# Optimization experiments

Hardware: AMD Instinct MI355X
Metric: run time of the kernel (lower is better)

The kernel has to match this reference:

```python
import jax, jax.numpy as jnp
import numpy as np

B, T, N, F, UNITS = 64, 12, 512, 64, 64

def setup_inputs() -> dict:
    key = jax.random.key(0)
    ks = jax.random.split(key, 9)
    inputs = jax.random.normal(ks[0], (B, T, N, F), dtype=jnp.float32)
    # binary k-hop adjacency mask with self loops (K.to_dense(calculate_adjacency_k(...)))
    A = (jax.random.uniform(ks[1], (N, N)) < 0.05).astype(jnp.float32)
    A = jnp.maximum(A, jnp.eye(N, dtype=jnp.float32))
    W1 = jax.random.normal(ks[2], (T, 1), dtype=jnp.float32) * 0.3
    W2 = jax.random.normal(ks[3], (F, T), dtype=jnp.float32) * 0.1
    W3 = jax.random.normal(ks[4], (F, 1), dtype=jnp.float32) * 0.1
    Ve = jax.random.normal(ks[5], (N, N), dtype=jnp.float32) * 0.05
    be = jax.random.normal(ks[6], (N, N), dtype=jnp.float32) * 0.05
    kernel = jax.random.normal(ks[7], (F, UNITS), dtype=jnp.float32) * 0.1
    bias = jax.random.normal(ks[8], (UNITS,), dtype=jnp.float32) * 0.1
    return {"inputs": inputs, "A": A, "W1": W1, "W2": W2, "W3": W3,
            "Ve": Ve, "be": be, "kernel": kernel, "bias": bias}

def reference(inputs, A, W1, W2, W3, Ve, be, kernel, bias):
    # inputs: (B, T, N, F)
    # lhs: permute->(B,N,F,T), dot W1, squeeze, dot W2 -> (B, N, T)
    r1 = jnp.einsum('btnf,t->bnf', inputs, W1[:, 0])
    lhs = jnp.einsum('bnf,ft->bnt', r1, W2)
    # rhs: dot W3, squeeze -> (B, T, N)
    rhs = jnp.einsum('btnf,f->btn', inputs, W3[:, 0])
    # batch_dot -> (B, N, N)
    product = jnp.einsum('bnt,btm->bnm', lhs, rhs)
    E = jnp.einsum('jk,bkm->bjm', Ve, jax.nn.sigmoid(product + be))
    masked = E + (-1e16) * (1.0 - A)            # adjacency mask
    attn = jax.nn.softmax(masked, axis=-1)       # (B, N, N)
    # graph conv: (B,N,N) x (B,T,N,F) -> (B,T,N,F)
    conv = jnp.einsum('bjk,btkf->btjf', attn, inputs)
    out = jnp.einsum('btjf,fu->btju', conv, kernel) + bias
    return out  # activation=None -> linear
```

## Files before the change

### kernel.cpp

```cpp
#include <hip/hip_runtime.h>
#include <hip/hip_bf16.h>
#include <cstdint>

constexpr int BB = 64;
constexpr int TT = 12;
constexpr int NN = 512;
constexpr int FF = 64;
constexpr int UU = 64;
constexpr int MAXNZ = 128;

constexpr size_t OF_LHS   = 0;
constexpr size_t OF_RHS   = 393216;
constexpr size_t OF_BET   = 786432;
constexpr size_t OF_EVALS = 1048576;
constexpr size_t OB_NNZ   = 20971520;
constexpr size_t OB_CIDX  = 20973568;
constexpr size_t OB_CCNT  = 21235712;
constexpr size_t OB_COLJ  = 21237760;
constexpr size_t OB_XT    = 21516288;
constexpr size_t XT_BYTES = (size_t)BB * NN * TT * FF * 2;
constexpr size_t OB_KF    = 71847936;
constexpr size_t KF_BYTES = 8 * 64 * 8 * 2;
constexpr size_t OB_VEB   = 71856128;
constexpr size_t VEB_BYTES = (size_t)NN * NN * 2;

typedef __attribute__((ext_vector_type(8))) short bf16x8;
typedef __attribute__((ext_vector_type(4))) float f32x4;

__device__ __forceinline__ float wred_sum(float v) {
  #pragma unroll
  for (int off = 32; off; off >>= 1) v += __shfl_xor(v, off, 64);
  return v;
}

__device__ __forceinline__ float bflo(unsigned u) {
  return __uint_as_float(u << 16);
}
__device__ __forceinline__ float bfhi(unsigned u) {
  return __uint_as_float(u & 0xFFFF0000u);
}

__global__ __launch_bounds__(256) void k_lhs_rhs(
    const float* __restrict__ x, const float* __restrict__ W1,
    const float* __restrict__ W2, const float* __restrict__ W3,
    float* __restrict__ lhs, float* __restrict__ rhsS,
    unsigned short* __restrict__ xT)
{
  int unit = blockIdx.x * 4 + (threadIdx.x >> 6);
  int lane = threadIdx.x & 63;
  int b = unit >> 9, n = unit & 511;

  const float* xb = x + ((size_t)b * TT * NN + n) * FF + lane;
  float xv[12];
  #pragma unroll
  for (int t = 0; t < 12; ++t) xv[t] = xb[(size_t)t * NN * FF];

  if (xT) {
    unsigned short* xo = xT + (size_t)unit * (TT * FF) + lane;
    #pragma unroll
    for (int t = 0; t < 12; ++t) {
      __hip_bfloat16 h = __float2bfloat16(xv[t]);
      xo[t * FF] = *reinterpret_cast<unsigned short*>(&h);
    }
  }

  float r1 = 0.f;
  #pragma unroll
  for (int t = 0; t < 12; ++t) r1 += xv[t] * W1[t];

  float w3 = W3[lane];

  float myl = 0.f, myr = 0.f;
  #pragma unroll
  for (int t = 0; t < 12; ++t) {
    float a = r1 * W2[lane * 12 + t];
    float c = xv[t] * w3;
    a = wred_sum(a);
    c = wred_sum(c);
    if (lane == t) { myl = a; myr = c; }
  }
  if (lane < 12) {
    lhs[(size_t)unit * 12 + lane]  = myl;
    rhsS[(size_t)unit * 12 + lane] = myr;
  }
}

__global__ __launch_bounds__(256) void k_transpose(
    const float* __restrict__ be, float* __restrict__ beT,
    const float* __restrict__ K, unsigned short* __restrict__ KF,
    const float* __restrict__ Ve, unsigned short* __restrict__ VeB)
{
  int bid = blockIdx.x;
  if (bid < NN * NN / 256) {
    int i = bid * 256 + threadIdx.x;
    int k = i >> 9, m = i & 511;
    beT[m * 512 + k] = be[i];
    return;
  }
  if (bid == NN * NN / 256) {
    if (KF) {
      for (int idx = threadIdx.x; idx < 512; idx += 256) {
        int frag = idx >> 6, l = idx & 63;
        int kk = frag >> 2, nt = frag & 3;
        int u = nt * 16 + (l & 15);
        unsigned short* dst = KF + (size_t)idx * 8;
        for (int e = 0; e < 8; ++e) {
          int f = kk * 32 + (l >> 4) * 8 + e;
          __hip_bfloat16 h = __float2bfloat16(K[f * 64 + u]);
          dst[e] = *reinterpret_cast<unsigned short*>(&h);
        }
      }
    }
    return;
  }
  if (VeB) {
    int b2 = bid - (NN * NN / 256 + 1);
    #pragma unroll
    for (int i = 0; i < 32; ++i) {
      int idx = b2 * 8192 + i * 256 + threadIdx.x;
      __hip_bfloat16 h = __float2bfloat16(Ve[idx]);
      VeB[idx] = *reinterpret_cast<unsigned short*>(&h);
    }
  }
}

__global__ void k_build_idx(const float* __restrict__ A,
                            int* __restrict__ nnz, int* __restrict__ cidx)
{
  int j = blockIdx.x;
  int lane = threadIdx.x;
  unsigned long long lt = (1ull << lane) - 1ull;
  int base = 0;
  for (int c = 0; c < 8; ++c) {
    int m = c * 64 + lane;
    bool p = A[(size_t)j * 512 + m] > 0.5f;
    unsigned long long mask = __ballot(p);
    int pos = base + __popcll(mask & lt);
    if (p && pos < MAXNZ) cidx[j * MAXNZ + pos] = m;
    base += __popcll(mask);
  }
  if (lane == 0) nnz[j] = base > MAXNZ ? MAXNZ : base;
}

__global__ void k_build_col(const int* __restrict__ nnz, const int* __restrict__ cidx,
                            int* __restrict__ ccnt, unsigned* __restrict__ colj)
{
  int j = blockIdx.x;
  int lane = threadIdx.x;
  int cnt = nnz[j];
  for (int s = lane; s < cnt; s += 64) {
    int m = cidx[j * MAXNZ + s];
    int pos = atomicAdd(&ccnt[m], 1);
    if (pos < MAXNZ) colj[m * MAXNZ + pos] = (unsigned)j | ((unsigned)s << 16);
  }
}

__global__ __launch_bounds__(256) void k_product_E6(
    const float* __restrict__ lhs, const float* __restrict__ rhsS,
    const float* __restrict__ beT, const unsigned short* __restrict__ VeB,
    const int* __restrict__ ccnt, const unsigned* __restrict__ colj,
    float* __restrict__ evals)
{
  int b  = blockIdx.x;
  int mc = blockIdx.y;

  __shared__ __align__(16) float sL[8][512];
  __shared__ float rh[8 * 12];

  int tid = threadIdx.x;
  int wave = tid >> 6, lane = tid & 63;
  int grp = lane >> 4, lg = lane & 15;

  float l0[12], l1[12];
  {
    const float* p0 = lhs + ((size_t)b * 512 + tid) * 12;
    const float* p1 = p0 + 256 * 12;
    #pragma unroll
    for (int t = 0; t < 12; ++t) { l0[t] = p0[t]; l1[t] = p1[t]; }
  }
  if (tid < 96) rh[tid] = rhsS[((size_t)b * 512 + mc * 8) * 12 + tid];
  __syncthreads();

  #pragma unroll
  for (int mm = 0; mm < 8; ++mm) {
    int m = mc * 8 + mm;
    float q0 = beT[m * 512 + tid];
    float q1 = beT[m * 512 + tid + 256];
    const float* rw = &rh[mm * 12];
    #pragma unroll
    for (int t = 0; t < 12; ++t) {
      q0 = fmaf(l0[t], rw[t], q0);
      q1 = fmaf(l1[t], rw[t], q1);
    }
    sL[mm][tid]       = 1.0f / (1.0f + __expf(-q0));
    sL[mm][tid + 256] = 1.0f / (1.0f + __expf(-q1));
  }
  __syncthreads();

  for (int cc = 0; cc < 2; ++cc) {
    int mm = wave + cc * 4;
    int m = mc * 8 + mm;
    int cnt = ccnt[m];
    if (cnt > MAXNZ) cnt = MAXNZ;
    const float4* sw4 = (const float4*)sL[mm];
    const unsigned* cj = colj + m * MAXNZ;

    int e0 = grp;
    for (; e0 + 4 < cnt; e0 += 8) {
      unsigned pk0 = cj[e0], pk1 = cj[e0 + 4];
      int j0 = pk0 & 0xffff, s0 = (int)(pk0 >> 16);
      int j1 = pk1 & 0xffff, s1 = (int)(pk1 >> 16);
      const uint2* va = (const uint2*)(VeB + (size_t)j0 * 512);
      const uint2* vb = (const uint2*)(VeB + (size_t)j1 * 512);
      float a = 0.f, c = 0.f;
      #pragma unroll
      for (int i = 0; i < 8; ++i) {
        float4 s4 = sw4[lg + 16 * i];
        uint2  u0 = va[lg + 16 * i];
        uint2  u1 = vb[lg + 16 * i];
        a = fmaf(bflo(u0.x), s4.x, a); a = fmaf(bfhi(u0.x), s4.y, a);
        a = fmaf(bflo(u0.y), s4.z, a); a = fmaf(bfhi(u0.y), s4.w, a);
        c = fmaf(bflo(u1.x), s4.x, c); c = fmaf(bfhi(u1.x), s4.y, c);
        c = fmaf(bflo(u1.y), s4.z, c); c = fmaf(bfhi(u1.y), s4.w, c);
      }
      #pragma unroll
      for (int off = 8; off; off >>= 1) {
        a += __shfl_xor(a, off, 64);
        c += __shfl_xor(c, off, 64);
      }
      if (lg == 0) {
        evals[((size_t)b * 512 + j0) * MAXNZ + s0] = a;
        evals[((size_t)b * 512 + j1) * MAXNZ + s1] = c;
      }
    }
    if (e0 < cnt) {
      unsigned pk0 = cj[e0];
      int j0 = pk0 & 0xffff, s0 = (int)(pk0 >> 16);
      const uint2* va = (const uint2*)(VeB + (size_t)j0 * 512);
      float a = 0.f;
      #pragma unroll
      for (int i = 0; i < 8; ++i) {
        float4 s4 = sw4[lg + 16 * i];
        uint2  u0 = va[lg + 16 * i];
        a = fmaf(bflo(u0.x), s4.x, a); a = fmaf(bfhi(u0.x), s4.y, a);
        a = fmaf(bflo(u0.y), s4.z, a); a = fmaf(bfhi(u0.y), s4.w, a);
      }
      #pragma unroll
      for (int off = 8; off; off >>= 1) a += __shfl_xor(a, off, 64);
      if (lg == 0) evals[((size_t)b * 512 + j0) * MAXNZ + s0] = a;
    }
  }
}

__global__ __launch_bounds__(256) void k_product_E5(
    const float* __restrict__ lhs, const float* __restrict__ rhsS,
    const float* __restrict__ beT, const float* __restrict__ Ve,
    const int* __restrict__ ccnt, const unsigned* __restrict__ colj,
    float* __restrict__ evals)
{
  int b  = blockIdx.x;
  int mc = blockIdx.y;

  __shared__ __align__(16) float sL[8][512];
  __shared__ float rh[8 * 12];

  int tid = threadIdx.x;
  int wave = tid >> 6, lane = tid & 63;
  int grp = lane >> 4, lg = lane & 15;

  float l0[12], l1[12];
  {
    const float* p0 = lhs + ((size_t)b * 512 + tid) * 12;
    const float* p1 = p0 + 256 * 12;
    #pragma unroll
    for (int t = 0; t < 12; ++t) { l0[t] = p0[t]; l1[t] = p1[t]; }
  }
  if (tid < 96) rh[tid] = rhsS[((size_t)b * 512 + mc * 8) * 12 + tid];
  __syncthreads();

  #pragma unroll
  for (int mm = 0; mm < 8; ++mm) {
    int m = mc * 8 + mm;
    float q0 = beT[m * 512 + tid];
    float q1 = beT[m * 512 + tid + 256];
    const float* rw = &rh[mm * 12];
    #pragma unroll
    for (int t = 0; t < 12; ++t) {
      q0 = fmaf(l0[t], rw[t], q0);
      q1 = fmaf(l1[t], rw[t], q1);
    }
    sL[mm][tid]       = 1.0f / (1.0f + __expf(-q0));
    sL[mm][tid + 256] = 1.0f / (1.0f + __expf(-q1));
  }
  __syncthreads();

  for (int cc = 0; cc < 2; ++cc) {
    int mm = wave + cc * 4;
    int m = mc * 8 + mm;
    int cnt = ccnt[m];
    if (cnt > MAXNZ) cnt = MAXNZ;
    const float4* sw4 = (const float4*)sL[mm];
    const unsigned* cj = colj + m * MAXNZ;

    int e0 = grp;
    for (; e0 + 4 < cnt; e0 += 8) {
      unsigned pk0 = cj[e0], pk1 = cj[e0 + 4];
      int j0 = pk0 & 0xffff, s0 = (int)(pk0 >> 16);
      int j1 = pk1 & 0xffff, s1 = (int)(pk1 >> 16);
      const float4* va = (const float4*)(Ve + (size_t)j0 * 512);
      const float4* vb = (const float4*)(Ve + (size_t)j1 * 512);
      float a = 0.f, c = 0.f;
      #pragma unroll
      for (int i = 0; i < 8; ++i) {
        float4 s4 = sw4[lg + 16 * i];
        float4 v4 = va[lg + 16 * i];
        float4 w4 = vb[lg + 16 * i];
        a = fmaf(v4.x, s4.x, a); a = fmaf(v4.y, s4.y, a);
        a = fmaf(v4.z, s4.z, a); a = fmaf(v4.w, s4.w, a);
        c = fmaf(w4.x, s4.x, c); c = fmaf(w4.y, s4.y, c);
        c = fmaf(w4.z, s4.z, c); c = fmaf(w4.w, s4.w, c);
      }
      #pragma unroll
      for (int off = 8; off; off >>= 1) {
        a += __shfl_xor(a, off, 64);
        c += __shfl_xor(c, off, 64);
      }
      if (lg == 0) {
        evals[((size_t)b * 512 + j0) * MAXNZ + s0] = a;
        evals[((size_t)b * 512 + j1) * MAXNZ + s1] = c;
      }
    }
    if (e0 < cnt) {
      unsigned pk0 = cj[e0];
      int j0 = pk0 & 0xffff, s0 = (int)(pk0 >> 16);
      const float4* va = (const float4*)(Ve + (size_t)j0 * 512);
      float a = 0.f;
      #pragma unroll
      for (int i = 0; i < 8; ++i) {
        float4 s4 = sw4[lg + 16 * i];
        float4 v4 = va[lg + 16 * i];
        a = fmaf(v4.x, s4.x, a); a = fmaf(v4.y, s4.y, a);
        a = fmaf(v4.z, s4.z, a); a = fmaf(v4.w, s4.w, a);
      }
      #pragma unroll
      for (int off = 8; off; off >>= 1) a += __shfl_xor(a, off, 64);
      if (lg == 0) evals[((size_t)b * 512 + j0) * MAXNZ + s0] = a;
    }
  }
}

__global__ __launch_bounds__(256) void k_out12(
    const unsigned short* __restrict__ xT,
    const int* __restrict__ nnz, const int* __restrict__ cidx,
    const float* __restrict__ evals,
    const unsigned short* __restrict__ KF, const float* __restrict__ bias,
    float* __restrict__ out)
{
  int tid = threadIdx.x;
  int wv = tid >> 6, lane = tid & 63;
  int bid = blockIdx.x;
  int sbid = (bid & 7) * 1024 + (bid >> 3);
  int unit = sbid * 4 + wv;
  int b = unit >> 9, j = unit & 511;

  __shared__ unsigned short convB[4][16][80];
  __shared__ float valL[4][MAXNZ];
  __shared__ int   idxL[4][MAXNZ];

  int cnt = nnz[j];
  for (int s = lane; s < cnt; s += 64) {
    idxL[wv][s] = cidx[j * MAXNZ + s];
    valL[wv][s] = evals[(size_t)unit * MAXNZ + s];
  }
  {
    float v0 = lane < cnt        ? valL[wv][lane]      : -__builtin_inff();
    float v1 = (lane + 64) < cnt ? valL[wv][lane + 64] : -__builtin_inff();
    float mx = fmaxf(v0, v1);
    #pragma unroll
    for (int off = 32; off; off >>= 1) mx = fmaxf(mx, __shfl_xor(mx, off, 64));
    float e0 = lane < cnt        ? __expf(v0 - mx) : 0.f;
    float e1 = (lane + 64) < cnt ? __expf(v1 - mx) : 0.f;
    float ssum = wred_sum(e0 + e1);
    float inv = 1.0f / ssum;
    if (lane < cnt)        valL[wv][lane]      = e0 * inv;
    if ((lane + 64) < cnt) valL[wv][lane + 64] = e1 * inv;
  }

  float2 acc[6];
  #pragma unroll
  for (int i = 0; i < 6; ++i) acc[i] = make_float2(0.f, 0.f);

  const unsigned* xb = reinterpret_cast<const unsigned*>(
      xT + (size_t)b * NN * (TT * FF));

  int s = 0;
  for (; s + 1 < cnt; s += 2) {
    int   k0 = idxL[wv][s],     k1 = idxL[wv][s + 1];
    float v0 = valL[wv][s],     v1 = valL[wv][s + 1];
    const unsigned* p0 = xb + k0 * 384 + lane;
    const unsigned* p1 = xb + k1 * 384 + lane;
    unsigned a0 = p0[0],   a1 = p0[64],  a2 = p0[128],
             a3 = p0[192], a4 = p0[256], a5 = p0[320];
    unsigned c0 = p1[0],   c1 = p1[64],  c2 = p1[128],
             c3 = p1[192], c4 = p1[256], c5 = p1[320];
    acc[0].x = fmaf(v0, bflo(a0), acc[0].x); acc[0].y = fmaf(v0, bfhi(a0), acc[0].y);
    acc[1].x = fmaf(v0, bflo(a1), acc[1].x); acc[1].y = fmaf(v0, bfhi(a1), acc[1].y);
    acc[2].x = fmaf(v0, bflo(a2), acc[2].x); acc[2].y = fmaf(v0, bfhi(a2), acc[2].y);
    acc[3].x = fmaf(v0, bflo(a3), acc[3].x); acc[3].y = fmaf(v0, bfhi(a3), acc[3].y);
    acc[4].x = fmaf(v0, bflo(a4), acc[4].x); acc[4].y = fmaf(v0, bfhi(a4), acc[4].y);
    acc[5].x = fmaf(v0, bflo(a5), acc[5].x); acc[5].y = fmaf(v0, bfhi(a5), acc[5].y);
    acc[0].x = fmaf(v1, bflo(c0), acc[0].x); acc[0].y = fmaf(v1, bfhi(c0), acc[0].y);
    acc[1].x = fmaf(v1, bflo(c1), acc[1].x); acc[1].y = fmaf(v1, bfhi(c1), acc[1].y);
    acc[2].x = fmaf(v1, bflo(c2), acc[2].x); acc[2].y = fmaf(v1, bfhi(c2), acc[2].y);
    acc[3].x = fmaf(v1, bflo(c3), acc[3].x); acc[3].y = fmaf(v1, bfhi(c3), acc[3].y);
    acc[4].x = fmaf(v1, bflo(c4), acc[4].x); acc[4].y = fmaf(v1, bfhi(c4), acc[4].y);
    acc[5].x = fmaf(v1, bflo(c5), acc[5].x); acc[5].y = fmaf(v1, bfhi(c5), acc[5].y);
  }
  if (s < cnt) {
    int   k0 = idxL[wv][s];
    float v0 = valL[wv][s];
    const unsigned* p0 = xb + k0 * 384 + lane;
    unsigned a0 = p0[0],   a1 = p0[64],  a2 = p0[128],
             a3 = p0[192], a4 = p0[256], a5 = p0[320];
    acc[0].x = fmaf(v0, bflo(a0), acc[0].x); acc[0].y = fmaf(v0, bfhi(a0), acc[0].y);
    acc[1].x = fmaf(v0, bflo(a1), acc[1].x); acc[1].y = fmaf(v0, bfhi(a1), acc[1].y);
    acc[2].x = fmaf(v0, bflo(a2), acc[2].x); acc[2].y = fmaf(v0, bfhi(a2), acc[2].y);
    acc[3].x = fmaf(v0, bflo(a3), acc[3].x); acc[3].y = fmaf(v0, bfhi(a3), acc[3].y);
    acc[4].x = fmaf(v0, bflo(a4), acc[4].x); acc[4].y = fmaf(v0, bfhi(a4), acc[4].y);
    acc[5].x = fmaf(v0, bflo(a5), acc[5].x); acc[5].y = fmaf(v0, bfhi(a5), acc[5].y);
  }

  int half = lane >> 5, fl = lane & 31;
  {
    unsigned short* cb = &convB[wv][0][0];
    #pragma unroll
    for (int i = 0; i < 6; ++i) {
      int t = 2 * i + half;
      __hip_bfloat16 hx = __float2bfloat16(acc[i].x);
      __hip_bfloat16 hy = __float2bfloat16(acc[i].y);
      unsigned pkd = (unsigned)*reinterpret_cast<unsigned short*>(&hx)
                   | ((unsigned)*reinterpret_cast<unsigned short*>(&hy) << 16);
      *reinterpret_cast<unsigned*>(&cb[t * 80 + fl * 2]) = pkd;
    }
  }

  int arow = lane & 15, agrp = lane >> 4;
  bf16x8 afrag0 = *reinterpret_cast<const bf16x8*>(&convB[wv][arow][agrp * 8]);
  bf16x8 afrag1 = *reinterpret_cast<const bf16x8*>(&convB[wv][arow][32 + agrp * 8]);
  const bf16x8* kf = reinterpret_cast<const bf16x8*>(KF);

  #pragma unroll
  for (int nt = 0; nt < 4; ++nt) {
    f32x4 accT = {0.f, 0.f, 0.f, 0.f};
    accT = __builtin_amdgcn_mfma_f32_16x16x32_bf16(afrag0, kf[(0 * 4 + nt) * 64 + lane], accT, 0, 0, 0);
    accT = __builtin_amdgcn_mfma_f32_16x16x32_bf16(afrag1, kf[(1 * 4 + nt) * 64 + lane], accT, 0, 0, 0);
    int u = nt * 16 + arow;
    float bb = bias[u];
    #pragma unroll
    for (int r = 0; r < 4; ++r) {
      int t = agrp * 4 + r;
      if (t < 12)
        out[((size_t)(b * TT + t) * NN + j) * UU + u] = accT[r] + bb;
    }
  }
}

__global__ __launch_bounds__(256) void k_out3f(
    const float* __restrict__ x,
    const int* __restrict__ nnz, const int* __restrict__ cidx,
    const float* __restrict__ evals,
    const float* __restrict__ K, const float* __restrict__ bias,
    float* __restrict__ out)
{
  int wv = threadIdx.x >> 6, lane = threadIdx.x & 63;
  int bid = blockIdx.x;
  int sbid = (bid & 7) * 1024 + (bid >> 3);
  int unit = sbid * 4 + wv;
  int b = unit >> 9, j = unit & 511;

  __shared__ float convL[4][12][64];
  __shared__ float valL[4][MAXNZ];
  __shared__ int   idxL[4][MAXNZ];

  int cnt = nnz[j];
  for (int s = lane; s < cnt; s += 64) {
    idxL[wv][s] = cidx[j * MAXNZ + s];
    valL[wv][s] = evals[(size_t)unit * MAXNZ + s];
  }
  {
    float v0 = lane < cnt        ? valL[wv][lane]      : -__builtin_inff();
    float v1 = (lane + 64) < cnt ? valL[wv][lane + 64] : -__builtin_inff();
    float mx = fmaxf(v0, v1);
    #pragma unroll
    for (int off = 32; off; off >>= 1) mx = fmaxf(mx, __shfl_xor(mx, off, 64));
    float e0 = lane < cnt        ? __expf(v0 - mx) : 0.f;
    float e1 = (lane + 64) < cnt ? __expf(v1 - mx) : 0.f;
    float ssum = wred_sum(e0 + e1);
    float inv = 1.0f / ssum;
    if (lane < cnt)        valL[wv][lane]      = e0 * inv;
    if ((lane + 64) < cnt) valL[wv][lane + 64] = e1 * inv;
  }

  float acc[12];
  #pragma unroll
  for (int t = 0; t < 12; ++t) acc[t] = 0.f;

  const float* xb = x + (size_t)b * TT * NN * FF + lane;
  for (int s = 0; s < cnt; ++s) {
    float v = valL[wv][s];
    const float* xk = xb + (size_t)idxL[wv][s] * FF;
    #pragma unroll
    for (int t = 0; t < 12; ++t)
      acc[t] = fmaf(v, xk[(size_t)t * NN * FF], acc[t]);
  }
  #pragma unroll
  for (int t = 0; t < 12; ++t) convL[wv][t][lane] = acc[t];

  float bs = bias[lane];
  float o[12];
  #pragma unroll
  for (int t = 0; t < 12; ++t) o[t] = bs;
  __syncthreads();

  #pragma unroll
  for (int ft = 0; ft < 4; ++ft) {
    float kc[16];
    #pragma unroll
    for (int i = 0; i < 16; ++i) kc[i] = K[(ft * 16 + i) * 64 + lane];
    #pragma unroll
    for (int t = 0; t < 12; ++t) {
      const float4* cv = (const float4*)&convL[wv][t][ft * 16];
      float4 c0 = cv[0], c1 = cv[1], c2 = cv[2], c3 = cv[3];
      float o_ = o[t];
      o_ = fmaf(c0.x, kc[0],  o_); o_ = fmaf(c0.y, kc[1],  o_);
      o_ = fmaf(c0.z, kc[2],  o_); o_ = fmaf(c0.w, kc[3],  o_);
      o_ = fmaf(c1.x, kc[4],  o_); o_ = fmaf(c1.y, kc[5],  o_);
      o_ = fmaf(c1.z, kc[6],  o_); o_ = fmaf(c1.w, kc[7],  o_);
      o_ = fmaf(c2.x, kc[8],  o_); o_ = fmaf(c2.y, kc[9],  o_);
      o_ = fmaf(c2.z, kc[10], o_); o_ = fmaf(c2.w, kc[11], o_);
      o_ = fmaf(c3.x, kc[12], o_); o_ = fmaf(c3.y, kc[13], o_);
      o_ = fmaf(c3.z, kc[14], o_); o_ = fmaf(c3.w, kc[15], o_);
      o[t] = o_;
    }
  }

  #pragma unroll
  for (int t = 0; t < 12; ++t)
    out[((size_t)(b * TT + t) * NN + j) * UU + lane] = o[t];
}

extern "C" void kernel_launch(void* const* d_in, const int* in_sizes, int n_in,
                              void* d_out, int out_size, void* d_ws, size_t ws_size,
                              hipStream_t stream)
{
  const float* x    = (const float*)d_in[0];
  const float* A    = (const float*)d_in[1];
  const float* W1   = (const float*)d_in[2];
  const float* W2   = (const float*)d_in[3];
  const float* W3   = (const float*)d_in[4];
  const float* Ve   = (const float*)d_in[5];
  const float* be   = (const float*)d_in[6];
  const float* K    = (const float*)d_in[7];
  const float* bias = (const float*)d_in[8];
  float* out = (float*)d_out;

  char* ws = (char*)d_ws;
  float* lhs   = (float*)ws + OF_LHS;
  float* rhsS  = (float*)ws + OF_RHS;
  float* beT   = (float*)ws + OF_BET;
  float* evals = (float*)ws + OF_EVALS;
  int*      nnz  = (int*)(ws + OB_NNZ);
  int*      cidx = (int*)(ws + OB_CIDX);
  int*      ccnt = (int*)(ws + OB_CCNT);
  unsigned* colj = (unsigned*)(ws + OB_COLJ);
  unsigned short* xT  = (unsigned short*)(ws + OB_XT);
  unsigned short* KF  = (unsigned short*)(ws + OB_KF);
  unsigned short* VeB = (unsigned short*)(ws + OB_VEB);

  const bool use_xt  = ws_size >= OB_KF + KF_BYTES;
  const bool use_veb = ws_size >= OB_VEB + VEB_BYTES;

  hipMemsetAsync(ccnt, 0, NN * sizeof(int), stream);

  k_lhs_rhs<<<dim3(BB * NN / 4), dim3(256), 0, stream>>>(
      x, W1, W2, W3, lhs, rhsS, use_xt ? xT : nullptr);
  k_transpose<<<dim3(NN * NN / 256 + 1 + (use_veb ? 32 : 0)), dim3(256), 0, stream>>>(
      be, beT, K, use_xt ? KF : nullptr, Ve, use_veb ? VeB : nullptr);
  k_build_idx<<<dim3(NN), dim3(64), 0, stream>>>(A, nnz, cidx);
  k_build_col<<<dim3(NN), dim3(64), 0, stream>>>(nnz, cidx, ccnt, colj);
  if (use_veb)
    k_product_E6<<<dim3(BB, NN / 8), dim3(256), 0, stream>>>(lhs, rhsS, beT, VeB, ccnt, colj, evals);
  else
    k_product_E5<<<dim3(BB, NN / 8), dim3(256), 0, stream>>>(lhs, rhsS, beT, Ve, ccnt, colj, evals);
  if (use_xt)
    k_out12<<<dim3(BB * NN / 4), dim3(256), 0, stream>>>(xT, nnz, cidx, evals, KF, bias, out);
  else
    k_out3f<<<dim3(BB * NN / 4), dim3(256), 0, stream>>>(x, nnz, cidx, evals, K, bias, out);
}
```

Before: 218.0 us.

## Split sigmoid and E computation, compute sparse E entries with bf16 MFMA

Replaces the fused product/E kernel with two kernels: one computes sigmoid(lhs·rhs + be) for all batches and writes it as a dense bf16 tensor, and a second computes only the adjacency-masked E entries per column m using bf16 MFMA over gathered Ve rows. The aim is to move the Ve contraction onto matrix cores and reuse each Ve row across all 64 batches within a block. In exchange it writes and rereads a 32 MB intermediate and needs a larger workspace. The path only runs when the workspace is big enough.

```diff
diff --git a/kernel.cpp b/kernel.cpp
--- a/kernel.cpp
+++ b/kernel.cpp
@@ -23,6 +23,8 @@
 constexpr size_t KF_BYTES = 8 * 64 * 8 * 2;
 constexpr size_t OB_VEB   = 71856128;
 constexpr size_t VEB_BYTES = (size_t)NN * NN * 2;
+constexpr size_t OB_ST    = 72380416;
+constexpr size_t ST_BYTES = (size_t)BB * NN * NN * 2;
 
 typedef __attribute__((ext_vector_type(8))) short bf16x8;
 typedef __attribute__((ext_vector_type(4))) float f32x4;
@@ -152,6 +154,115 @@
     int m = cidx[j * MAXNZ + s];
     int pos = atomicAdd(&ccnt[m], 1);
     if (pos < MAXNZ) colj[m * MAXNZ + pos] = (unsigned)j | ((unsigned)s << 16);
+  }
+}
+
+__global__ __launch_bounds__(256) void k_sigmoid2(
+    const float* __restrict__ lhs, const float* __restrict__ rhsS,
+    const float* __restrict__ beT, unsigned short* __restrict__ ST)
+{
+  int b  = blockIdx.x;
+  int mc = blockIdx.y;
+
+  __shared__ float rh[16 * 12];
+  int tid = threadIdx.x;
+
+  float l0[12], l1[12];
+  {
+    const float* p0 = lhs + ((size_t)b * 512 + tid) * 12;
+    const float* p1 = p0 + 256 * 12;
+    #pragma unroll
+    for (int t = 0; t < 12; ++t) { l0[t] = p0[t]; l1[t] = p1[t]; }
+  }
+  if (tid < 192) rh[tid] = rhsS[((size_t)b * 512 + mc * 16) * 12 + tid];
+  __syncthreads();
+
+  #pragma unroll 4
+  for (int mm = 0; mm < 16; ++mm) {
+    int m = mc * 16 + mm;
+    float q0 = beT[m * 512 + tid];
+    float q1 = beT[m * 512 + tid + 256];
+    const float* rw = &rh[mm * 12];
+    #pragma unroll
+    for (int t = 0; t < 12; ++t) {
+      q0 = fmaf(l0[t], rw[t], q0);
+      q1 = fmaf(l1[t], rw[t], q1);
+    }
+    float s0 = 1.0f / (1.0f + __expf(-q0));
+    float s1 = 1.0f / (1.0f + __expf(-q1));
+    __hip_bfloat16 h0 = __float2bfloat16(s0);
+    __hip_bfloat16 h1 = __float2bfloat16(s1);
+    unsigned short* dst = ST + ((size_t)(b * NN + m)) * NN;
+    dst[tid]       = *reinterpret_cast<unsigned short*>(&h0);
+    dst[tid + 256] = *reinterpret_cast<unsigned short*>(&h1);
+  }
+}
+
+__global__ __launch_bounds__(256) void k_E_mfma(
+    const unsigned short* __restrict__ ST, const unsigned short* __restrict__ VeB,
+    const int* __restrict__ ccnt, const unsigned* __restrict__ colj,
+    float* __restrict__ evals)
+{
+  int m = blockIdx.x;
+  int tid = threadIdx.x;
+  int wv = tid >> 6, lane = tid & 63;
+  int arow = lane & 15, kgrp = lane >> 4;
+
+  __shared__ unsigned short VeL[32][520];
+  __shared__ unsigned entL[MAXNZ];
+
+  int cnt = ccnt[m];
+  if (cnt > MAXNZ) cnt = MAXNZ;
+  for (int e = tid; e < cnt; e += 256) entL[e] = colj[m * MAXNZ + e];
+
+  bf16x8 bfrag[16];
+  {
+    const unsigned short* sb =
+        ST + ((size_t)((wv * 16 + arow) * NN + m)) * NN + kgrp * 8;
+    #pragma unroll
+    for (int kk = 0; kk < 16; ++kk)
+      bfrag[kk] = *reinterpret_cast<const bf16x8*>(sb + kk * 32);
+  }
+
+  for (int c0 = 0; c0 < cnt; c0 += 32) {
+    __syncthreads();
+    {
+      int r = tid >> 3, seg = tid & 7;
+      int e = c0 + r;
+      uint2* dst = reinterpret_cast<uint2*>(&VeL[r][0]);
+      if (e < cnt) {
+        unsigned jrow = entL[e] & 0xffffu;
+        const uint2* src = reinterpret_cast<const uint2*>(VeB + (size_t)jrow * 512);
+        #pragma unroll
+        for (int i = 0; i < 16; ++i) dst[seg + 8 * i] = src[seg + 8 * i];
+      } else {
+        uint2 z = make_uint2(0u, 0u);
+        #pragma unroll
+        for (int i = 0; i < 16; ++i) dst[seg + 8 * i] = z;
+      }
+    }
+    __syncthreads();
+
+    int b = wv * 16 + arow;
+    #pragma unroll
+    for (int jt = 0; jt < 2; ++jt) {
+      f32x4 acc = {0.f, 0.f, 0.f, 0.f};
+      #pragma unroll
+      for (int kk = 0; kk < 16; ++kk) {
+        bf16x8 af = *reinterpret_cast<const bf16x8*>(
+            &VeL[jt * 16 + arow][kgrp * 8 + kk * 32]);
+        acc = __builtin_amdgcn_mfma_f32_16x16x32_bf16(af, bfrag[kk], acc, 0, 0, 0);
+      }
+      #pragma unroll
+      for (int r = 0; r < 4; ++r) {
+        int e = c0 + jt * 16 + kgrp * 4 + r;
+        if (e < cnt) {
+          unsigned pk = entL[e];
+          int j = pk & 0xffff, slot = (int)(pk >> 16);
+          evals[((size_t)b * 512 + j) * MAXNZ + slot] = acc[r];
+        }
+      }
+    }
   }
 }
 
@@ -576,9 +687,11 @@
   unsigned short* xT  = (unsigned short*)(ws + OB_XT);
   unsigned short* KF  = (unsigned short*)(ws + OB_KF);
   unsigned short* VeB = (unsigned short*)(ws + OB_VEB);
-
-  const bool use_xt  = ws_size >= OB_KF + KF_BYTES;
-  const bool use_veb = ws_size >= OB_VEB + VEB_BYTES;
+  unsigned short* ST  = (unsigned short*)(ws + OB_ST);
+
+  const bool use_xt    = ws_size >= OB_KF + KF_BYTES;
+  const bool use_veb   = ws_size >= OB_VEB + VEB_BYTES;
+  const bool use_mfmaE = ws_size >= OB_ST + ST_BYTES;
 
   hipMemsetAsync(ccnt, 0, NN * sizeof(int), stream);
 
@@ -588,10 +701,14 @@
       be, beT, K, use_xt ? KF : nullptr, Ve, use_veb ? VeB : nullptr);
   k_build_idx<<<dim3(NN), dim3(64), 0, stream>>>(A, nnz, cidx);
   k_build_col<<<dim3(NN), dim3(64), 0, stream>>>(nnz, cidx, ccnt, colj);
-  if (use_veb)
+  if (use_mfmaE && use_veb) {
+    k_sigmoid2<<<dim3(BB, NN / 16), dim3(256), 0, stream>>>(lhs, rhsS, beT, ST);
+    k_E_mfma<<<dim3(NN), dim3(256), 0, stream>>>(ST, VeB, ccnt, colj, evals);
+  } else if (use_veb) {
     k_product_E6<<<dim3(BB, NN / 8), dim3(256), 0, stream>>>(lhs, rhsS, beT, VeB, ccnt, colj, evals);
-  else
+  } else {
     k_product_E5<<<dim3(BB, NN / 8), dim3(256), 0, stream>>>(lhs, rhsS, beT, Ve, ccnt, colj, evals);
+  }
   if (use_xt)
     k_out12<<<dim3(BB * NN / 4), dim3(256), 0, stream>>>(xT, nnz, cidx, evals, KF, bias, out);
   else
```

Result: faster. 181.2 us (median of 3 runs) (-16.9%).
